# Kernel tuning notes

Hardware: AMD Instinct MI355X
Metric: run time of the kernel (lower is better)

The kernel has to match this reference:

```python
import jax, jax.numpy as jnp
import numpy as np

N = 200000
E = 5000000


def _gcn_norm(edge_index, num_nodes):
    # add self-loops and compute symmetric normalization (PyG GCNConv default)
    loop = jnp.arange(num_nodes, dtype=edge_index.dtype)
    src = jnp.concatenate([edge_index[0], loop])
    dst = jnp.concatenate([edge_index[1], loop])
    ones = jnp.ones(dst.shape[0], dtype=jnp.float32)
    deg = jax.ops.segment_sum(ones, dst, num_segments=num_nodes)
    dis = jnp.where(deg > 0, jax.lax.rsqrt(deg), 0.0)
    norm = dis[src] * dis[dst]  # [E+N]
    return src, dst, norm


def _gcn_layer(x, src, dst, norm, W, b, num_nodes):
    xl = x @ W  # [N, out] dense linear (no bias, PyG default)
    msg = xl[src] * norm[:, None]  # gather + scale
    agg = jax.ops.segment_sum(msg, dst, num_segments=num_nodes)  # scatter-add
    return agg + b


def setup_inputs() -> dict:
    key = jax.random.key(0)
    ks = jax.random.split(key, 10)
    x = jax.random.normal(ks[0], (N, 12), dtype=jnp.float32)
    edge_index = jax.random.randint(ks[1], (2, E), 0, N, dtype=jnp.int64)
    def glorot(k, fi, fo):
        s = np.sqrt(6.0 / (fi + fo)).astype(np.float32)
        return jax.random.uniform(k, (fi, fo), jnp.float32, -s, s)
    return {
        "x": x,
        "edge_index": edge_index,
        "W1": glorot(ks[2], 12, 16), "b1": jnp.zeros((16,), jnp.float32),
        "W2": glorot(ks[3], 16, 8), "b2": jnp.zeros((8,), jnp.float32),
        "W3": glorot(ks[4], 8, 16), "b3": jnp.zeros((16,), jnp.float32),
        "W4": glorot(ks[5], 16, 12), "b4": jnp.zeros((12,), jnp.float32),
    }


def reference(x, edge_index, W1, b1, W2, b2, W3, b3, W4, b4):
    num_nodes = x.shape[0]
    src, dst, norm = _gcn_norm(edge_index, num_nodes)
    # Encoder
    h = jax.nn.relu(_gcn_layer(x, src, dst, norm, W1, b1, num_nodes))
    h = _gcn_layer(h, src, dst, norm, W2, b2, num_nodes)
    # Decoder
    h = jax.nn.relu(_gcn_layer(h, src, dst, norm, W3, b3, num_nodes))
    h = jax.nn.sigmoid(_gcn_layer(h, src, dst, norm, W4, b4, num_nodes))
    return h
```

## Files before the change

### kernel.cpp

```cpp
#include <hip/hip_runtime.h>
#include <hip/hip_fp16.h>
#include <math.h>


#define NPB 1024
#define MAX_NB 256
#define CAP 26496
#define BIN_CHUNK 4096
#define BIN_TH 512
#define EPT (BIN_CHUNK / BIN_TH)
#define MAXB CAP

__global__ void init_cur_kernel(int* __restrict__ bucket_cur, int NB) {
    int t = blockIdx.x * blockDim.x + threadIdx.x;
    if (t < NB) bucket_cur[t] = t * CAP;
}

__global__ __launch_bounds__(BIN_TH) void bin_kernel(const int* __restrict__ src,
                                                     const int* __restrict__ dst,
                                                     int* __restrict__ bucket_cur,
                                                     unsigned int* __restrict__ binned,
                                                     int E, int NB) {
    __shared__ int h[MAX_NB];
    __shared__ int scl[MAX_NB + 1];
    __shared__ int base[MAX_NB];
    __shared__ int sscan[256];
    __shared__ unsigned int stage[BIN_CHUNK];
    __shared__ unsigned char bkt8[BIN_CHUNK];
    int cbeg = blockIdx.x * BIN_CHUNK;
    int cend = min(cbeg + BIN_CHUNK, E);
    int chunk_n = cend - cbeg;
    int tid = threadIdx.x;

    for (int t = tid; t < NB; t += BIN_TH) h[t] = 0;
    __syncthreads();
    int myd[EPT];
#pragma unroll
    for (int j = 0; j < EPT; j++) {
        int e = cbeg + tid + j * BIN_TH;
        if (e < cend) {
            myd[j] = dst[e];
            atomicAdd(&h[myd[j] >> 10], 1);
        }
    }
    __syncthreads();
    int v = (tid < NB) ? h[tid] : 0;
    if (tid < 256) sscan[tid] = v;
    __syncthreads();
    for (int off = 1; off < 256; off <<= 1) {
        int t = (tid >= off && tid < 256) ? sscan[tid - off] : 0;
        __syncthreads();
        if (tid < 256) sscan[tid] += t;
        __syncthreads();
    }
    if (tid < NB) {
        scl[tid] = sscan[tid] - v;
        base[tid] = v ? atomicAdd(&bucket_cur[tid], v) : 0;
    }
    if (tid == 0) scl[NB] = chunk_n;
    __syncthreads();
    for (int t = tid; t < NB; t += BIN_TH) h[t] = 0;
    __syncthreads();
#pragma unroll
    for (int j = 0; j < EPT; j++) {
        int e = cbeg + tid + j * BIN_TH;
        if (e < cend) {
            int d = myd[j];
            int bkt = d >> 10;
            int pos = scl[bkt] + atomicAdd(&h[bkt], 1);
            stage[pos] = ((unsigned)src[e] << 10) | (unsigned)(d & 1023);
            bkt8[pos] = (unsigned char)bkt;
        }
    }
    __syncthreads();
    for (int k = tid; k < chunk_n; k += BIN_TH) {
        int bkt = bkt8[k];
        binned[base[bkt] + (k - scl[bkt])] = stage[k];
    }
}

__global__ __launch_bounds__(1024) void csr_bucket_t1_kernel(
    const unsigned int* __restrict__ binned,
    const int* __restrict__ bucket_cur,
    int2* __restrict__ rows, float* __restrict__ dis,
    int* __restrict__ col,
    const float* __restrict__ x, const float* __restrict__ W1,
    __half* __restrict__ xls, int N) {
    __shared__ int cnt[NPB];
    __shared__ int cur[NPB];
    __shared__ int colbuf[MAXB];
    __shared__ float sW[12 * 16];
    int b = blockIdx.x;
    int nbase = b << 10;
    int nlocal = min(NPB, N - nbase);
    int beg = b * CAP;
    int bsize = bucket_cur[b] - beg;
    int tid = threadIdx.x;

    if (tid < 192) sW[tid] = W1[tid];
    cnt[tid] = 0;
    __syncthreads();
    for (int k = tid; k < bsize; k += 1024)
        atomicAdd(&cnt[binned[beg + k] & 1023u], 1);
    __syncthreads();
    int v = cnt[tid];
    cur[tid] = v;
    __syncthreads();
    for (int off = 1; off < 1024; off <<= 1) {
        int t = (tid >= off) ? cur[tid - off] : 0;
        __syncthreads();
        cur[tid] += t;
        __syncthreads();
    }
    int excl = cur[tid] - v;
    float d = 1.0f / sqrtf((float)(v + 1));
    if (tid < nlocal) {
        rows[nbase + tid] = make_int2(beg + excl, beg + excl + v);
        dis[nbase + tid] = d;
    }
    __syncthreads();
    cur[tid] = excl;
    __syncthreads();
    if (bsize <= MAXB) {
        for (int k = tid; k < bsize; k += 1024) {
            unsigned rec = binned[beg + k];
            int pos = atomicAdd(&cur[rec & 1023u], 1);
            colbuf[pos] = (int)(rec >> 10);
        }
        __syncthreads();
        for (int k = tid; k < bsize; k += 1024) col[beg + k] = colbuf[k];
    } else {
        for (int k = tid; k < bsize; k += 1024) {
            unsigned rec = binned[beg + k];
            int pos = atomicAdd(&cur[rec & 1023u], 1);
            col[beg + pos] = (int)(rec >> 10);
        }
    }
    if (tid < nlocal) {
        int i = nbase + tid;
        float h[12];
#pragma unroll
        for (int k = 0; k < 12; k++) h[k] = x[(size_t)i * 12 + k];
        float o[16];
#pragma unroll
        for (int f = 0; f < 16; f++) {
            float acc = 0.0f;
#pragma unroll
            for (int k = 0; k < 12; k++) acc = fmaf(h[k], sW[k * 16 + f], acc);
            o[f] = acc * d;
        }
        __half2* x2 = (__half2*)xls;
#pragma unroll
        for (int c = 0; c < 2; c++) {
#pragma unroll
            for (int k = 0; k < 4; k++) {
                x2[(size_t)c * N * 4 + (size_t)i * 4 + k] =
                    __floats2half2_rn(o[c * 8 + 2 * k], o[c * 8 + 2 * k + 1]);
            }
        }
    }
}

template <int IN, int OUT, int C, int PREACT, bool SPLITIN>
__global__ __launch_bounds__(256) void transform_kernel(
    const float* __restrict__ hin0, const float* __restrict__ hin1,
    const float* __restrict__ bias_prev,
    const float* __restrict__ W, const float* __restrict__ dis,
    __half* __restrict__ xls, int N) {
    __shared__ float sW[IN * OUT];
    __shared__ float sB[IN];
    for (int t = threadIdx.x; t < IN * OUT; t += blockDim.x) sW[t] = W[t];
    if (PREACT != 0) {
        for (int t = threadIdx.x; t < IN; t += blockDim.x) sB[t] = bias_prev[t];
    }
    __syncthreads();
    int i = blockIdx.x * blockDim.x + threadIdx.x;
    if (i >= N) return;

    constexpr int CIN = SPLITIN ? IN / 2 : IN;
    float h[IN];
#pragma unroll
    for (int k = 0; k < IN; k++) {
        float v;
        if (SPLITIN)
            v = (k < CIN) ? hin0[(size_t)i * CIN + k]
                          : hin1[(size_t)i * CIN + (k - CIN)];
        else
            v = hin0[(size_t)i * IN + k];
        if (PREACT != 0) {
            v += sB[k];
            if (PREACT == 1) v = fmaxf(v, 0.0f);
        }
        h[k] = v;
    }
    float d = dis[i];
    float o[OUT];
#pragma unroll
    for (int f = 0; f < OUT; f++) {
        float acc = 0.0f;
#pragma unroll
        for (int k = 0; k < IN; k++) acc = fmaf(h[k], sW[k * OUT + f], acc);
        o[f] = acc * d;
    }
    constexpr int NCH = OUT / C;
    constexpr int P = C / 2;
    __half2* x2 = (__half2*)xls;
#pragma unroll
    for (int c = 0; c < NCH; c++) {
#pragma unroll
        for (int k = 0; k < P; k++) {
            x2[(size_t)c * N * P + (size_t)i * P + k] =
                __floats2half2_rn(o[c * C + 2 * k], o[c * C + 2 * k + 1]);
        }
    }
}

template <int P>
__device__ __forceinline__ void acc_node(const __half2* __restrict__ x2, int c,
                                         float2 (&acc)[P]) {
    __half2 t[P];
#pragma unroll
    for (int k = 0; k < P; k++) t[k] = x2[(size_t)c * P + k];
#pragma unroll
    for (int k = 0; k < P; k++) {
        float2 v = __half22float2(t[k]);
        acc[k].x += v.x;
        acc[k].y += v.y;
    }
}

template <int P>
__device__ __forceinline__ void acc_quad(const __half2* __restrict__ x2, int4 c,
                                         float2 (&acc)[P]) {
    __half2 t[4][P];
#pragma unroll
    for (int k = 0; k < P; k++) t[0][k] = x2[(size_t)c.x * P + k];
#pragma unroll
    for (int k = 0; k < P; k++) t[1][k] = x2[(size_t)c.y * P + k];
#pragma unroll
    for (int k = 0; k < P; k++) t[2][k] = x2[(size_t)c.z * P + k];
#pragma unroll
    for (int k = 0; k < P; k++) t[3][k] = x2[(size_t)c.w * P + k];
#pragma unroll
    for (int k = 0; k < P; k++) {
        float2 a0 = __half22float2(t[0][k]), a1 = __half22float2(t[1][k]);
        float2 a2 = __half22float2(t[2][k]), a3 = __half22float2(t[3][k]);
        acc[k].x += (a0.x + a1.x) + (a2.x + a3.x);
        acc[k].y += (a0.y + a1.y) + (a2.y + a3.y);
    }
}

template <int C>
__device__ __forceinline__ void gather_acc(
    int i, int p, const int2* __restrict__ rows, const int* __restrict__ col,
    const __half2* __restrict__ x2, float2 (&acc)[C / 2]) {
    constexpr int P = C / 2;
#pragma unroll
    for (int k = 0; k < P; k++) {
        if (p == 0) acc[k] = __half22float2(x2[(size_t)i * P + k]);
        else acc[k] = make_float2(0.0f, 0.0f);
    }
    int2 r = rows[i];
    int beg = r.x;
    int end = r.y;
    int nedge = end - beg;
    int pre = (4 - (beg & 3)) & 3;
    if (pre > nedge) pre = nedge;
    for (int j = p; j < pre; j += 2) acc_node<P>(x2, col[beg + j], acc);
    int abeg = beg + pre;
    int nq = (end - abeg) >> 2;
    int q = p;
    for (; q + 4 < nq; q += 6) {
        int4 ca = *reinterpret_cast<const int4*>(col + abeg + 4 * q);
        int4 cb = *reinterpret_cast<const int4*>(col + abeg + 4 * (q + 2));
        int4 cc = *reinterpret_cast<const int4*>(col + abeg + 4 * (q + 4));
        acc_quad<P>(x2, ca, acc);
        acc_quad<P>(x2, cb, acc);
        acc_quad<P>(x2, cc, acc);
    }
    for (; q < nq; q += 2) {
        int4 ca = *reinterpret_cast<const int4*>(col + abeg + 4 * q);
        acc_quad<P>(x2, ca, acc);
    }
    int tbeg = abeg + 4 * nq;
    for (int j = tbeg + p; j < end; j += 2) acc_node<P>(x2, col[j], acc);
#pragma unroll
    for (int k = 0; k < P; k++) {
        acc[k].x += __shfl_xor(acc[k].x, 1);
        acc[k].y += __shfl_xor(acc[k].y, 1);
    }
}

template <int C>
__global__ __launch_bounds__(256) void gather2_kernel(
    const int2* __restrict__ rows, const int* __restrict__ col,
    const float* __restrict__ dis, const __half* __restrict__ x0,
    const __half* __restrict__ x1, float* __restrict__ agg0,
    float* __restrict__ agg1, int N) {
    constexpr int P = C / 2;
    int grp = blockIdx.x >> 3;
    int sub = blockIdx.x & 7;
    int chunk = sub >> 2;
    int range = (grp << 2) + (sub & 3);
    int t2 = range * 256 + (int)threadIdx.x;
    int i = t2 >> 1;
    int p = t2 & 1;
    if (i >= N) return;
    const __half2* x2 = (const __half2*)(chunk ? x1 : x0);
    float* aggc = chunk ? agg1 : agg0;
    float2 acc[P];
    gather_acc<C>(i, p, rows, col, x2, acc);
    float d = dis[i];
    float2* ap = (float2*)(aggc + (size_t)i * C);
#pragma unroll
    for (int k = 0; k < P; k++) {
        if ((k & 1) == p) ap[k] = make_float2(acc[k].x * d, acc[k].y * d);
    }
}

__global__ __launch_bounds__(256) void gather_t3_kernel(
    const int2* __restrict__ rows, const int* __restrict__ col,
    const float* __restrict__ dis, const __half* __restrict__ xls,
    const float* __restrict__ b2, const float* __restrict__ W3,
    __half* __restrict__ xout, int N) {
    __shared__ float sW[8 * 16];
    __shared__ float sB[8];
    if (threadIdx.x < 128) sW[threadIdx.x] = W3[threadIdx.x];
    if (threadIdx.x < 8) sB[threadIdx.x] = b2[threadIdx.x];
    __syncthreads();
    int tid = blockIdx.x * blockDim.x + threadIdx.x;
    int i = tid >> 1;
    int p = tid & 1;
    if (i >= N) return;
    float2 acc[4];
    gather_acc<8>(i, p, rows, col, (const __half2*)xls, acc);
    float d = dis[i];
    float v[8];
#pragma unroll
    for (int k = 0; k < 4; k++) {
        v[2 * k] = acc[k].x * d + sB[2 * k];
        v[2 * k + 1] = acc[k].y * d + sB[2 * k + 1];
    }
    float o[8];
#pragma unroll
    for (int f = 0; f < 8; f++) {
        float a = 0.0f;
#pragma unroll
        for (int k = 0; k < 8; k++) a = fmaf(v[k], sW[k * 16 + p * 8 + f], a);
        o[f] = a * d;
    }
    __half2* x2o = (__half2*)xout;
#pragma unroll
    for (int k = 0; k < 4; k++) {
        x2o[(size_t)p * N * 4 + (size_t)i * 4 + k] =
            __floats2half2_rn(o[2 * k], o[2 * k + 1]);
    }
}

__global__ __launch_bounds__(256) void gather2_sig_kernel(
    const int2* __restrict__ rows, const int* __restrict__ col,
    const float* __restrict__ dis, const __half* __restrict__ x0,
    const __half* __restrict__ x1, const float* __restrict__ bias,
    float* __restrict__ out, int N) {
    int grp = blockIdx.x >> 3;
    int sub = blockIdx.x & 7;
    int chunk = sub >> 2;
    int range = (grp << 2) + (sub & 3);
    int t2 = range * 256 + (int)threadIdx.x;
    int i = t2 >> 1;
    int p = t2 & 1;
    if (i >= N) return;
    const __half2* x2 = (const __half2*)(chunk ? x1 : x0);
    int coff = chunk ? 6 : 0;
    float2 acc[3];
    gather_acc<6>(i, p, rows, col, x2, acc);
    float d = dis[i];
    float* op = out + (size_t)i * 12 + coff;
#pragma unroll
    for (int k = 0; k < 3; k++) {
        if ((k & 1) == p) {
            float vx = 1.0f / (1.0f + expf(-(acc[k].x * d + bias[coff + 2 * k])));
            float vy = 1.0f / (1.0f + expf(-(acc[k].y * d + bias[coff + 2 * k + 1])));
            *reinterpret_cast<float2*>(op + 2 * k) = make_float2(vx, vy);
        }
    }
}

static inline size_t align_up(size_t v, size_t a) { return (v + a - 1) & ~(a - 1); }

extern "C" void kernel_launch(void* const* d_in, const int* in_sizes, int n_in,
                              void* d_out, int out_size, void* d_ws, size_t ws_size,
                              hipStream_t stream) {
    const float* x  = (const float*)d_in[0];
    const int*   ei = (const int*)d_in[1];
    const float* W1 = (const float*)d_in[2];
    const float* b1 = (const float*)d_in[3];
    const float* W2 = (const float*)d_in[4];
    const float* b2 = (const float*)d_in[5];
    const float* W3 = (const float*)d_in[6];
    const float* b3 = (const float*)d_in[7];
    const float* W4 = (const float*)d_in[8];
    const float* b4 = (const float*)d_in[9];
    float* out = (float*)d_out;

    const int N = in_sizes[0] / 12;
    const int E = in_sizes[1] / 2;
    const int* src = ei;
    const int* dst = ei + E;
    const int NB = (N + NPB - 1) / NPB;

    char* ws = (char*)d_ws;
    size_t off = 0;
    int* bucket_cur = (int*)(ws + off);   off = align_up(off + (size_t)NB * 4, 256);
    int2* rows = (int2*)(ws + off);       off = align_up(off + (size_t)N * 8, 256);
    float* dis = (float*)(ws + off);      off = align_up(off + (size_t)N * 4, 256);
    unsigned int* binned = (unsigned int*)(ws + off);
    off = align_up(off + ((size_t)NB * CAP + 4096) * 4, 256);
    int* col = (int*)(ws + off);          off = align_up(off + ((size_t)NB * CAP + 4096) * 4, 256);
    __half* xls = (__half*)(ws + off);    off = align_up(off + (size_t)N * 16 * 2, 256);
    __half* xls2 = (__half*)(ws + off);   off = align_up(off + (size_t)N * 16 * 2, 256);
    float* aggA = (float*)(ws + off);     off = align_up(off + (size_t)N * 16 * 4, 256);
    (void)ws_size; (void)n_in; (void)out_size;

    const int B = 256;
    auto blocks = [&](long long n) { return (int)((n + B - 1) / B); };
    int nb2 = blocks(2LL * N);
    nb2 = (nb2 + 3) & ~3;
    const int G2 = nb2 * 2;

    init_cur_kernel<<<1, 256, 0, stream>>>(bucket_cur, NB);
    bin_kernel<<<(E + BIN_CHUNK - 1) / BIN_CHUNK, BIN_TH, 0, stream>>>(src, dst, bucket_cur, binned, E, NB);
    csr_bucket_t1_kernel<<<NB, 1024, 0, stream>>>(binned, bucket_cur, rows, dis, col,
                                                  x, W1, xls, N);

    __half* x_c0 = xls;
    __half* x_c8 = xls + (size_t)N * 8;
    __half* x_c6 = xls + (size_t)N * 6;
    __half* x2_c0 = xls2;
    __half* x2_c8 = xls2 + (size_t)N * 8;
    float* aggA0 = aggA;
    float* aggA1 = aggA + (size_t)N * 8;

    gather2_kernel<8><<<G2, B, 0, stream>>>(rows, col, dis, x_c0, x_c8, aggA0, aggA1, N);

    transform_kernel<16, 8, 8, 1, true><<<blocks(N), B, 0, stream>>>(
        aggA0, aggA1, b1, W2, dis, xls, N);

    gather_t3_kernel<<<blocks(2LL * N), B, 0, stream>>>(rows, col, dis, x_c0,
                                                        b2, W3, xls2, N);

    gather2_kernel<8><<<G2, B, 0, stream>>>(rows, col, dis, x2_c0, x2_c8, aggA0, aggA1, N);

    transform_kernel<16, 12, 6, 1, true><<<blocks(N), B, 0, stream>>>(
        aggA0, aggA1, b3, W4, dis, xls, N);

    gather2_sig_kernel<<<G2, B, 0, stream>>>(rows, col, dis, x_c0, x_c6, b4, out, N);
}
```

Measured before the change: 398.8 us.

## Reorder GCN aggregation and linear transforms to gather at narrowest width

```diff
diff --git a/kernel.cpp b/kernel.cpp
--- a/kernel.cpp
+++ b/kernel.cpp
@@ -84,12 +84,11 @@
     const int* __restrict__ bucket_cur,
     int2* __restrict__ rows, float* __restrict__ dis,
     int* __restrict__ col,
-    const float* __restrict__ x, const float* __restrict__ W1,
+    const float* __restrict__ x,
     __half* __restrict__ xls, int N) {
     __shared__ int cnt[NPB];
     __shared__ int cur[NPB];
     __shared__ int colbuf[MAXB];
-    __shared__ float sW[12 * 16];
     int b = blockIdx.x;
     int nbase = b << 10;
     int nlocal = min(NPB, N - nbase);
@@ -97,7 +96,6 @@
     int bsize = bucket_cur[b] - beg;
     int tid = threadIdx.x;
 
-    if (tid < 192) sW[tid] = W1[tid];
     cnt[tid] = 0;
     __syncthreads();
     for (int k = tid; k < bsize; k += 1024)
@@ -141,76 +139,14 @@
         float h[12];
 #pragma unroll
         for (int k = 0; k < 12; k++) h[k] = x[(size_t)i * 12 + k];
-        float o[16];
-#pragma unroll
-        for (int f = 0; f < 16; f++) {
-            float acc = 0.0f;
-#pragma unroll
-            for (int k = 0; k < 12; k++) acc = fmaf(h[k], sW[k * 16 + f], acc);
-            o[f] = acc * d;
-        }
         __half2* x2 = (__half2*)xls;
 #pragma unroll
         for (int c = 0; c < 2; c++) {
 #pragma unroll
-            for (int k = 0; k < 4; k++) {
-                x2[(size_t)c * N * 4 + (size_t)i * 4 + k] =
-                    __floats2half2_rn(o[c * 8 + 2 * k], o[c * 8 + 2 * k + 1]);
+            for (int k = 0; k < 3; k++) {
+                x2[(size_t)c * N * 3 + (size_t)i * 3 + k] =
+                    __floats2half2_rn(h[6 * c + 2 * k] * d, h[6 * c + 2 * k + 1] * d);
             }
-        }
-    }
-}
-
-template <int IN, int OUT, int C, int PREACT, bool SPLITIN>
-__global__ __launch_bounds__(256) void transform_kernel(
-    const float* __restrict__ hin0, const float* __restrict__ hin1,
-    const float* __restrict__ bias_prev,
-    const float* __restrict__ W, const float* __restrict__ dis,
-    __half* __restrict__ xls, int N) {
-    __shared__ float sW[IN * OUT];
-    __shared__ float sB[IN];
-    for (int t = threadIdx.x; t < IN * OUT; t += blockDim.x) sW[t] = W[t];
-    if (PREACT != 0) {
-        for (int t = threadIdx.x; t < IN; t += blockDim.x) sB[t] = bias_prev[t];
-    }
-    __syncthreads();
-    int i = blockIdx.x * blockDim.x + threadIdx.x;
-    if (i >= N) return;
-
-    constexpr int CIN = SPLITIN ? IN / 2 : IN;
-    float h[IN];
-#pragma unroll
-    for (int k = 0; k < IN; k++) {
-        float v;
-        if (SPLITIN)
-            v = (k < CIN) ? hin0[(size_t)i * CIN + k]
-                          : hin1[(size_t)i * CIN + (k - CIN)];
-        else
-            v = hin0[(size_t)i * IN + k];
-        if (PREACT != 0) {
-            v += sB[k];
-            if (PREACT == 1) v = fmaxf(v, 0.0f);
-        }
-        h[k] = v;
-    }
-    float d = dis[i];
-    float o[OUT];
-#pragma unroll
-    for (int f = 0; f < OUT; f++) {
-        float acc = 0.0f;
-#pragma unroll
-        for (int k = 0; k < IN; k++) acc = fmaf(h[k], sW[k * OUT + f], acc);
-        o[f] = acc * d;
-    }
-    constexpr int NCH = OUT / C;
-    constexpr int P = C / 2;
-    __half2* x2 = (__half2*)xls;
-#pragma unroll
-    for (int c = 0; c < NCH; c++) {
-#pragma unroll
-        for (int k = 0; k < P; k++) {
-            x2[(size_t)c * N * P + (size_t)i * P + k] =
-                __floats2half2_rn(o[c * C + 2 * k], o[c * C + 2 * k + 1]);
         }
     }
 }
@@ -318,42 +254,118 @@
     }
 }
 
-__global__ __launch_bounds__(256) void gather_t3_kernel(
+__global__ __launch_bounds__(256) void transform12_kernel(
+    const float* __restrict__ a0, const float* __restrict__ a1,
+    const float* __restrict__ b1, const float* __restrict__ W1,
+    const float* __restrict__ W2, const float* __restrict__ dis,
+    __half* __restrict__ xout, int N) {
+    __shared__ float sW1[12 * 16];
+    __shared__ float sW2[16 * 8];
+    __shared__ float sB[16];
+    if (threadIdx.x < 192) sW1[threadIdx.x] = W1[threadIdx.x];
+    if (threadIdx.x < 128) sW2[threadIdx.x] = W2[threadIdx.x];
+    if (threadIdx.x < 16) sB[threadIdx.x] = b1[threadIdx.x];
+    __syncthreads();
+    int i = blockIdx.x * blockDim.x + threadIdx.x;
+    if (i >= N) return;
+    float A[12];
+#pragma unroll
+    for (int k = 0; k < 6; k++) {
+        A[k] = a0[(size_t)i * 6 + k];
+        A[6 + k] = a1[(size_t)i * 6 + k];
+    }
+    float h[16];
+#pragma unroll
+    for (int f = 0; f < 16; f++) {
+        float acc = sB[f];
+#pragma unroll
+        for (int k = 0; k < 12; k++) acc = fmaf(A[k], sW1[k * 16 + f], acc);
+        h[f] = fmaxf(acc, 0.0f);
+    }
+    float d = dis[i];
+    __half2* x2 = (__half2*)xout;
+#pragma unroll
+    for (int k2 = 0; k2 < 4; k2++) {
+        float o0 = 0.0f, o1 = 0.0f;
+#pragma unroll
+        for (int k = 0; k < 16; k++) {
+            o0 = fmaf(h[k], sW2[k * 8 + 2 * k2], o0);
+            o1 = fmaf(h[k], sW2[k * 8 + 2 * k2 + 1], o1);
+        }
+        x2[(size_t)i * 4 + k2] = __floats2half2_rn(o0 * d, o1 * d);
+    }
+}
+
+__global__ __launch_bounds__(256) void gather8_t3_kernel(
     const int2* __restrict__ rows, const int* __restrict__ col,
-    const float* __restrict__ dis, const __half* __restrict__ xls,
-    const float* __restrict__ b2, const float* __restrict__ W3,
-    __half* __restrict__ xout, int N) {
-    __shared__ float sW[8 * 16];
-    __shared__ float sB[8];
-    if (threadIdx.x < 128) sW[threadIdx.x] = W3[threadIdx.x];
-    if (threadIdx.x < 8) sB[threadIdx.x] = b2[threadIdx.x];
-    __syncthreads();
+    const float* __restrict__ dis, const __half* __restrict__ xin,
+    const float* __restrict__ b2, __half* __restrict__ xout, int N) {
     int tid = blockIdx.x * blockDim.x + threadIdx.x;
     int i = tid >> 1;
     int p = tid & 1;
     if (i >= N) return;
     float2 acc[4];
-    gather_acc<8>(i, p, rows, col, (const __half2*)xls, acc);
+    gather_acc<8>(i, p, rows, col, (const __half2*)xin, acc);
     float d = dis[i];
-    float v[8];
+    __half2* x2o = (__half2*)xout;
 #pragma unroll
     for (int k = 0; k < 4; k++) {
-        v[2 * k] = acc[k].x * d + sB[2 * k];
-        v[2 * k + 1] = acc[k].y * d + sB[2 * k + 1];
-    }
-    float o[8];
+        if ((k >> 1) == p) {
+            x2o[(size_t)i * 4 + k] =
+                __floats2half2_rn((acc[k].x * d + b2[2 * k]) * d,
+                                  (acc[k].y * d + b2[2 * k + 1]) * d);
+        }
+    }
+}
+
+__global__ __launch_bounds__(256) void gather8_t4_kernel(
+    const int2* __restrict__ rows, const int* __restrict__ col,
+    const float* __restrict__ dis, const __half* __restrict__ xin,
+    const float* __restrict__ b3, const float* __restrict__ W3,
+    const float* __restrict__ W4, __half* __restrict__ xout, int N) {
+    __shared__ float sW3[8 * 16];
+    __shared__ float sW4[16 * 12];
+    __shared__ float sB[16];
+    if (threadIdx.x < 128) sW3[threadIdx.x] = W3[threadIdx.x];
+    if (threadIdx.x < 192) sW4[threadIdx.x] = W4[threadIdx.x];
+    if (threadIdx.x < 16) sB[threadIdx.x] = b3[threadIdx.x];
+    __syncthreads();
+    int tid = blockIdx.x * blockDim.x + threadIdx.x;
+    int i = tid >> 1;
+    int p = tid & 1;
+    if (i >= N) return;
+    float2 acc[4];
+    gather_acc<8>(i, p, rows, col, (const __half2*)xin, acc);
+    float d = dis[i];
+    float A[8];
+#pragma unroll
+    for (int k = 0; k < 4; k++) {
+        A[2 * k] = acc[k].x * d;
+        A[2 * k + 1] = acc[k].y * d;
+    }
+    float h[8];
 #pragma unroll
     for (int f = 0; f < 8; f++) {
+        float a = sB[p * 8 + f];
+#pragma unroll
+        for (int k = 0; k < 8; k++) a = fmaf(A[k], sW3[k * 16 + p * 8 + f], a);
+        h[f] = fmaxf(a, 0.0f);
+    }
+    float o[12];
+#pragma unroll
+    for (int j = 0; j < 12; j++) {
         float a = 0.0f;
 #pragma unroll
-        for (int k = 0; k < 8; k++) a = fmaf(v[k], sW[k * 16 + p * 8 + f], a);
-        o[f] = a * d;
-    }
+        for (int f = 0; f < 8; f++) a = fmaf(h[f], sW4[(p * 8 + f) * 12 + j], a);
+        o[j] = a;
+    }
+#pragma unroll
+    for (int j = 0; j < 12; j++) o[j] += __shfl_xor(o[j], 1);
     __half2* x2o = (__half2*)xout;
 #pragma unroll
-    for (int k = 0; k < 4; k++) {
-        x2o[(size_t)p * N * 4 + (size_t)i * 4 + k] =
-            __floats2half2_rn(o[2 * k], o[2 * k + 1]);
+    for (int k = 0; k < 3; k++) {
+        x2o[(size_t)p * N * 3 + (size_t)i * 3 + k] =
+            __floats2half2_rn(o[6 * p + 2 * k] * d, o[6 * p + 2 * k + 1] * d);
     }
 }
 
@@ -431,28 +443,23 @@
     init_cur_kernel<<<1, 256, 0, stream>>>(bucket_cur, NB);
     bin_kernel<<<(E + BIN_CHUNK - 1) / BIN_CHUNK, BIN_TH, 0, stream>>>(src, dst, bucket_cur, binned, E, NB);
     csr_bucket_t1_kernel<<<NB, 1024, 0, stream>>>(binned, bucket_cur, rows, dis, col,
-                                                  x, W1, xls, N);
+                                                  x, xls, N);
 
     __half* x_c0 = xls;
-    __half* x_c8 = xls + (size_t)N * 8;
     __half* x_c6 = xls + (size_t)N * 6;
-    __half* x2_c0 = xls2;
-    __half* x2_c8 = xls2 + (size_t)N * 8;
+    __half* t4_c0 = xls2;
+    __half* t4_c6 = xls2 + (size_t)N * 6;
     float* aggA0 = aggA;
-    float* aggA1 = aggA + (size_t)N * 8;
-
-    gather2_kernel<8><<<G2, B, 0, stream>>>(rows, col, dis, x_c0, x_c8, aggA0, aggA1, N);
-
-    transform_kernel<16, 8, 8, 1, true><<<blocks(N), B, 0, stream>>>(
-        aggA0, aggA1, b1, W2, dis, xls, N);
-
-    gather_t3_kernel<<<blocks(2LL * N), B, 0, stream>>>(rows, col, dis, x_c0,
-                                                        b2, W3, xls2, N);
-
-    gather2_kernel<8><<<G2, B, 0, stream>>>(rows, col, dis, x2_c0, x2_c8, aggA0, aggA1, N);
-
-    transform_kernel<16, 12, 6, 1, true><<<blocks(N), B, 0, stream>>>(
-        aggA0, aggA1, b3, W4, dis, xls, N);
-
-    gather2_sig_kernel<<<G2, B, 0, stream>>>(rows, col, dis, x_c0, x_c6, b4, out, N);
-}
+    float* aggA1 = aggA + (size_t)N * 6;
+
+    gather2_kernel<6><<<G2, B, 0, stream>>>(rows, col, dis, x_c0, x_c6, aggA0, aggA1, N);
+
+    transform12_kernel<<<blocks(N), B, 0, stream>>>(aggA0, aggA1, b1, W1, W2, dis, xls2, N);
+
+    gather8_t3_kernel<<<blocks(2LL * N), B, 0, stream>>>(rows, col, dis, xls2, b2, xls, N);
+
+    gather8_t4_kernel<<<blocks(2LL * N), B, 0, stream>>>(rows, col, dis, xls, b3, W3, W4,
+                                                         xls2, N);
+
+    gather2_sig_kernel<<<G2, B, 0, stream>>>(rows, col, dis, t4_c0, t4_c6, b4, out, N);
+}
```

Result: faster. 358.2 us (-10.2%).
